# Optimization experiments

Measured on AMD Instinct MI355X. Metric: run time of the kernel, lower is better.

## Reference

```python
import jax, jax.numpy as jnp
import numpy as np

BS, C_IN, L = 64, 64, 4096
C_OUT, KS, K, RATIO = 128, 7, 4, 4
HIDDEN = C_IN // RATIO
PAD, TEMP = 3, 30.0


def setup_inputs() -> dict:
    key = jax.random.key(0)
    k1, k2, k3, k4, k5 = jax.random.split(key, 5)
    x = jax.random.normal(k1, (BS, C_IN, L), dtype=jnp.float32)
    # attention 1x1 convs stored as matmul matrices
    w_attn1 = jax.random.normal(k2, (HIDDEN, C_IN), dtype=jnp.float32) * (2.0 / C_IN) ** 0.5
    w_attn2 = jax.random.normal(k3, (K, HIDDEN), dtype=jnp.float32) * (2.0 / HIDDEN) ** 0.5
    # K-bank conv weights [K, out, in, ks] and biases [K, out]
    weight = jax.random.normal(k4, (K, C_OUT, C_IN, KS), dtype=jnp.float32) * 0.05
    bias = jax.random.normal(k5, (K, C_OUT), dtype=jnp.float32) * 0.05
    return {"x": x, "w_attn1": w_attn1, "w_attn2": w_attn2, "weight": weight, "bias": bias}


def reference(x, w_attn1, w_attn2, weight, bias):
    # Attention1d: global avg pool -> 1x1 conv -> relu -> 1x1 conv -> softmax(./T)
    pooled = jnp.mean(x, axis=-1)                      # [bs, C_in]
    h = jax.nn.relu(pooled @ w_attn1.T)                # [bs, hidden]
    logits = h @ w_attn2.T                             # [bs, K]
    att = jax.nn.softmax(logits / TEMP, axis=-1)       # [bs, K]

    # softmax-weighted aggregation of the K weight banks -> per-sample kernels
    agg_w = jnp.einsum('bk,koif->boif', att, weight)   # [bs, out, in, ks]
    agg_b = att @ bias                                 # [bs, out]

    # per-sample conv1d (the grouped-conv trick), vectorized with vmap
    def conv_one(xi, wi):
        # xi: [C_in, L], wi: [out, in, ks]
        return jax.lax.conv_general_dilated(
            xi[None], wi, window_strides=(1,), padding=[(PAD, PAD)],
            dimension_numbers=('NCH', 'OIH', 'NCH'))[0]  # [out, L]

    out = jax.vmap(conv_one)(x, agg_w) + agg_b[:, :, None]  # [bs, out, L]
    return out
```

## Files before the change

kernel.cpp:

```cpp
#include <hip/hip_runtime.h>

typedef __bf16 bf16;
typedef __bf16 bf16x8 __attribute__((ext_vector_type(8)));
typedef __bf16 bf16x2 __attribute__((ext_vector_type(2)));
typedef float f32x4 __attribute__((ext_vector_type(4)));

#define BS 64
#define CI 64
#define LEN 4096
#define CO 128
#define KS 7
#define NK 4
#define HID 16
#define TEMP 30.0f

#define KTOT 448
#define WROW 456
#define WBAT (CO * WROW)
#define LTILE 128
#define TPB 8
#define XB_ROWS 4112
#define XB_ELE (XB_ROWS * 64)
#define NPART 16

__device__ __forceinline__ void gl_lds16(const void* g, void* l) {
    auto gp = reinterpret_cast<const __attribute__((address_space(1))) unsigned int*>(
        reinterpret_cast<unsigned long long>(g));
    auto lp = reinterpret_cast<__attribute__((address_space(3))) unsigned int*>(
        reinterpret_cast<unsigned long long>(l));
    __builtin_amdgcn_global_load_lds(gp, lp, 16, 0, 0);
}

__global__ __launch_bounds__(256) void trans_kernel(const float* __restrict__ x,
                                                    bf16* __restrict__ xbf,
                                                    float* __restrict__ part) {
    int bid = blockIdx.x;
    int b = bid >> 4, lt = bid & 15;
    int t = threadIdx.x;
    int si = t >> 2, sf = t & 3;
    __shared__ __align__(16) bf16 lds_t[128 * 72];
    __shared__ float lds_red[64 * 4];

    const float* xb = x + (size_t)b * CI * LEN;
    bf16* xo = xbf + (size_t)b * XB_ELE;
    float psum = 0.f;
    int ls0 = lt * 256;

    float4 v0[8], v1[8];
#pragma unroll
    for (int j = 0; j < 8; ++j)
        v0[j] = *(const float4*)(xb + (size_t)si * LEN + ls0 + 4 * (sf + 4 * j));
#pragma unroll
    for (int j = 0; j < 8; ++j)
        v1[j] = *(const float4*)(xb + (size_t)si * LEN + ls0 + 128 + 4 * (sf + 4 * j));

#pragma unroll
    for (int st = 0; st < 2; ++st) {
        const float4* v = st ? v1 : v0;
        int ls = ls0 + st * 128;
#pragma unroll
        for (int j = 0; j < 8; ++j) {
            float4 vv = v[j];
            psum += (vv.x + vv.y) + (vv.z + vv.w);
#pragma unroll
            for (int e = 0; e < 4; ++e)
                lds_t[(4 * (sf + 4 * j) + e) * 72 + si] = (bf16)((&vv.x)[e]);
        }
        __syncthreads();
        int row = t >> 3, l8 = t & 7;
#pragma unroll
        for (int pass = 0; pass < 4; ++pass) {
            int r = pass * 32 + row;
            int gl = ls + r + 8;
            uint4 d = *(const uint4*)((const char*)lds_t + r * 144 + l8 * 16);
            int sw = l8 ^ (gl & 7);
            *(uint4*)((char*)xo + (size_t)gl * 128 + sw * 16) = d;
        }
        if (st == 0) __syncthreads();
    }

    lds_red[si * 4 + sf] = psum;
    __syncthreads();
    if (t < 64)
        part[((size_t)b * NPART + lt) * 64 + t] =
            lds_red[t * 4] + lds_red[t * 4 + 1] + lds_red[t * 4 + 2] + lds_red[t * 4 + 3];

    if (lt == 0 && t < 128) *(uint2*)((char*)xo + t * 8) = make_uint2(0u, 0u);
    if (lt == 15 && t < 128) *(uint2*)((char*)xo + (size_t)4104 * 128 + t * 8) = make_uint2(0u, 0u);
}

__global__ void aggw_kernel(const float* __restrict__ part,
                            const float* __restrict__ w1,
                            const float* __restrict__ w2,
                            const float* __restrict__ weight,
                            float* __restrict__ att_g,
                            bf16* __restrict__ wagg) {
    int o = blockIdx.x >> 1;
    int bh = blockIdx.x & 1;
    int t = threadIdx.x;
    __shared__ float p[32 * 64];
    __shared__ float hsh[32 * 16];
    __shared__ float att_s[32][4];
    __shared__ float lw[4 * KTOT];

    const float* wo = weight + (size_t)o * KTOT;
    for (int idx = t; idx < 4 * KTOT; idx += 256) {
        int bank = idx / KTOT;
        int r = idx - bank * KTOT;
        lw[idx] = wo[(size_t)bank * (CO * KTOT) + r];
    }
    for (int idx = t; idx < 32 * 64; idx += 256) {
        int bb = idx >> 6, i = idx & 63;
        const float* pp = part + ((size_t)(bh * 32 + bb) * NPART) * 64 + i;
        float s = 0.f;
#pragma unroll
        for (int j = 0; j < NPART; ++j) s += pp[j * 64];
        p[idx] = s * (1.0f / LEN);
    }
    __syncthreads();

    {
        int bb = t >> 3, h2 = (t & 7) * 2;
#pragma unroll
        for (int u = 0; u < 2; ++u) {
            int hh = h2 + u;
            float s = 0.f;
            for (int i = 0; i < 64; ++i) s += p[bb * 64 + i] * w1[hh * 64 + i];
            hsh[bb * 16 + hh] = fmaxf(s, 0.f);
        }
    }
    __syncthreads();
    if (t < 32) {
        float lg[NK], m = -1e30f;
#pragma unroll
        for (int k = 0; k < NK; ++k) {
            float s = 0.f;
            for (int j = 0; j < HID; ++j) s += hsh[t * 16 + j] * w2[k * HID + j];
            lg[k] = s * (1.0f / TEMP);
            m = fmaxf(m, lg[k]);
        }
        float e[NK], tot = 0.f;
#pragma unroll
        for (int k = 0; k < NK; ++k) { e[k] = expf(lg[k] - m); tot += e[k]; }
        float inv = 1.0f / tot;
#pragma unroll
        for (int k = 0; k < NK; ++k) {
            att_s[t][k] = e[k] * inv;
            if (blockIdx.x < 2) att_g[(bh * 32 + t) * NK + k] = e[k] * inv;
        }
    }
    __syncthreads();

    if (t < 224) {
        float w8[8];
#pragma unroll
        for (int j = 0; j < 2; ++j) {
            int kout = 2 * t + j;
            int i = kout & 63, f = kout >> 6;
#pragma unroll
            for (int bank = 0; bank < 4; ++bank)
                w8[j * 4 + bank] = lw[bank * KTOT + i * KS + f];
        }
        for (int bb = 0; bb < 32; ++bb) {
            int b = bh * 32 + bb;
            float a0 = att_s[bb][0], a1 = att_s[bb][1];
            float a2 = att_s[bb][2], a3 = att_s[bb][3];
            float v0 = a0 * w8[0] + a1 * w8[1] + a2 * w8[2] + a3 * w8[3];
            float v1 = a0 * w8[4] + a1 * w8[5] + a2 * w8[6] + a3 * w8[7];
            bf16x2 pk; pk[0] = (bf16)v0; pk[1] = (bf16)v1;
            *(bf16x2*)(wagg + (size_t)b * WBAT + o * WROW + 2 * t) = pk;
        }
    }
}

__global__ __launch_bounds__(256, 2) void conv_kernel(
    const bf16* __restrict__ xbf,
    const bf16* __restrict__ wagg,
    const float* __restrict__ att_g,
    const float* __restrict__ bias,
    float* __restrict__ out) {
    __shared__ __align__(1024) bf16 lds_x[2][144 * 64];
    __shared__ float aggb_l[CO];

    int nwg = gridDim.x;
    int bid = blockIdx.x;
    int logical = (bid & 7) * (nwg >> 3) + (bid >> 3);
    int b = logical >> 3;
    int rem = logical & 7;
    int oh = rem >> 2, lsp = rem & 3;

    int t = threadIdx.x;
    int lane = t & 63, wid = t >> 6;
    int ln = lane & 15, g = lane >> 4;
    int wm = wid >> 1, wn = wid & 1;

    if (t < CO) {
        float a0 = att_g[b * NK + 0], a1 = att_g[b * NK + 1];
        float a2 = att_g[b * NK + 2], a3 = att_g[b * NK + 3];
        aggb_l[t] = a0 * bias[0 * CO + t] + a1 * bias[1 * CO + t] +
                    a2 * bias[2 * CO + t] + a3 * bias[3 * CO + t];
    }

    const bf16* wgb = wagg + (size_t)b * WBAT
                    + (size_t)(oh * 64 + wm * 32 + ln) * WROW + g * 8;
    bf16x8 av[2][14];
#pragma unroll
    for (int mf = 0; mf < 2; ++mf)
#pragma unroll
        for (int kk = 0; kk < 14; ++kk)
            av[mf][kk] = *(const bf16x8*)(wgb + mf * 16 * WROW + kk * 32);

    int l0base = lsp * (LTILE * TPB);
    const bf16* xb = xbf + (size_t)b * XB_ELE;

    auto stage = [&](int buf, int l0) {
        const char* src = (const char*)xb + (size_t)l0 * 128 + lane * 16;
        char* dst = (char*)lds_x[buf];
        for (int c = wid; c < 18; c += 4)
            gl_lds16(src + c * 1024, dst + c * 1024);
    };

    stage(0, l0base);
    __syncthreads();

    float bias_r[2][4];
    int orow_off[2][4];
#pragma unroll
    for (int mf = 0; mf < 2; ++mf)
#pragma unroll
        for (int r = 0; r < 4; ++r) {
            int o = oh * 64 + wm * 32 + mf * 16 + g * 4 + r;
            bias_r[mf][r] = aggb_l[o];
            orow_off[mf][r] = (b * CO + o) * LEN;
        }

    int prow = wn * 64 + ln + 5;

    for (int tl = 0; tl < TPB; ++tl) {
        int l0 = l0base + tl * LTILE;
        if (tl + 1 < TPB) stage((tl + 1) & 1, l0 + LTILE);

        f32x4 acc[2][4];
#pragma unroll
        for (int mf = 0; mf < 2; ++mf)
#pragma unroll
            for (int nf = 0; nf < 4; ++nf)
                acc[mf][nf] = (f32x4){0.f, 0.f, 0.f, 0.f};

        const char* lb = (const char*)lds_x[tl & 1];

#pragma unroll
        for (int kk = 0; kk < 14; ++kk) {
            int f = kk >> 1;
            int key = (prow + f) & 7;
            int swz = (((kk & 1) * 4 + g) ^ key) * 16;
            bf16x8 bv[4];
#pragma unroll
            for (int nf = 0; nf < 4; ++nf)
                bv[nf] = *(const bf16x8*)(lb + (prow + nf * 16 + f) * 128 + swz);
#pragma unroll
            for (int mf = 0; mf < 2; ++mf)
#pragma unroll
                for (int nf = 0; nf < 4; ++nf)
                    acc[mf][nf] = __builtin_amdgcn_mfma_f32_16x16x32_bf16(
                        av[mf][kk], bv[nf], acc[mf][nf], 0, 0, 0);
        }

        if (tl + 1 < TPB) __syncthreads();

#pragma unroll
        for (int mf = 0; mf < 2; ++mf)
#pragma unroll
            for (int nf = 0; nf < 4; ++nf) {
                int l = l0 + wn * 64 + nf * 16 + ln;
#pragma unroll
                for (int r = 0; r < 4; ++r)
                    out[(size_t)orow_off[mf][r] + l] = acc[mf][nf][r] + bias_r[mf][r];
            }
    }
}

extern "C" void kernel_launch(void* const* d_in, const int* in_sizes, int n_in,
                              void* d_out, int out_size, void* d_ws, size_t ws_size,
                              hipStream_t stream) {
    const float* x  = (const float*)d_in[0];
    const float* w1 = (const float*)d_in[1];
    const float* w2 = (const float*)d_in[2];
    const float* wt = (const float*)d_in[3];
    const float* bs = (const float*)d_in[4];
    float* out = (float*)d_out;

    bf16* xbf    = (bf16*)d_ws;
    bf16* wagg   = (bf16*)((char*)d_ws + (size_t)BS * XB_ELE * 2);
    float* part  = (float*)((char*)wagg + (size_t)BS * WBAT * 2);
    float* att_g = part + BS * NPART * 64;

    trans_kernel<<<BS * 16, 256, 0, stream>>>(x, xbf, part);
    aggw_kernel<<<CO * 2, 256, 0, stream>>>(part, w1, w2, wt, att_g, wagg);
    conv_kernel<<<BS * 8, 256, 0, stream>>>(xbf, wagg, att_g, bs, out);
}
```

Baseline: 66.85 us.

## Give each wave private LDS double buffers and drop block barriers in conv

Each wave now stages only the input rows it needs (72 rows) into its own double buffer. Completion is tracked with explicit vmcnt waits instead of block-wide __syncthreads, and the bias aggregation moves from shared memory into per-thread registers. The goal is to remove barrier stalls and let waves run independently, at the cost of overlapping halos being loaded twice across waves and a larger LDS footprint (72KB), which may limit occupancy to two blocks per CU. The hand-tuned vmcnt counts must match the exact number of outstanding loads, or the kernel will read incomplete data.

```diff
diff --git a/kernel.cpp b/kernel.cpp
--- a/kernel.cpp
+++ b/kernel.cpp
@@ -17,8 +17,6 @@
 #define KTOT 448
 #define WROW 456
 #define WBAT (CO * WROW)
-#define LTILE 128
-#define TPB 8
 #define XB_ROWS 4112
 #define XB_ELE (XB_ROWS * 64)
 #define NPART 16
@@ -179,8 +177,7 @@
     const float* __restrict__ att_g,
     const float* __restrict__ bias,
     float* __restrict__ out) {
-    __shared__ __align__(1024) bf16 lds_x[2][144 * 64];
-    __shared__ float aggb_l[CO];
+    __shared__ __align__(1024) bf16 lds_x[4][2][4608];
 
     int nwg = gridDim.x;
     int bid = blockIdx.x;
@@ -194,13 +191,6 @@
     int ln = lane & 15, g = lane >> 4;
     int wm = wid >> 1, wn = wid & 1;
 
-    if (t < CO) {
-        float a0 = att_g[b * NK + 0], a1 = att_g[b * NK + 1];
-        float a2 = att_g[b * NK + 2], a3 = att_g[b * NK + 3];
-        aggb_l[t] = a0 * bias[0 * CO + t] + a1 * bias[1 * CO + t] +
-                    a2 * bias[2 * CO + t] + a3 * bias[3 * CO + t];
-    }
-
     const bf16* wgb = wagg + (size_t)b * WBAT
                     + (size_t)(oh * 64 + wm * 32 + ln) * WROW + g * 8;
     bf16x8 av[2][14];
@@ -210,35 +200,45 @@
         for (int kk = 0; kk < 14; ++kk)
             av[mf][kk] = *(const bf16x8*)(wgb + mf * 16 * WROW + kk * 32);
 
-    int l0base = lsp * (LTILE * TPB);
-    const bf16* xb = xbf + (size_t)b * XB_ELE;
-
-    auto stage = [&](int buf, int l0) {
-        const char* src = (const char*)xb + (size_t)l0 * 128 + lane * 16;
-        char* dst = (char*)lds_x[buf];
-        for (int c = wid; c < 18; c += 4)
+    float a0 = att_g[b * NK + 0], a1 = att_g[b * NK + 1];
+    float a2 = att_g[b * NK + 2], a3 = att_g[b * NK + 3];
+    float bias_r[2][4];
+    size_t orow[2][4];
+#pragma unroll
+    for (int mf = 0; mf < 2; ++mf)
+#pragma unroll
+        for (int r = 0; r < 4; ++r) {
+            int o = oh * 64 + wm * 32 + mf * 16 + g * 4 + r;
+            bias_r[mf][r] = a0 * bias[o] + a1 * bias[CO + o] +
+                            a2 * bias[2 * CO + o] + a3 * bias[3 * CO + o];
+            orow[mf][r] = ((size_t)(b * CO + o)) * LEN;
+        }
+
+    int l0base = lsp * 1024;
+    int l0w = l0base + wn * 64;
+    const char* xbb = (const char*)(xbf + (size_t)b * XB_ELE);
+    char* buf0 = (char*)&lds_x[wid][0][0];
+    char* buf1 = (char*)&lds_x[wid][1][0];
+
+    auto stage = [&](char* dst, int gl0) {
+        const char* src = xbb + (size_t)gl0 * 128 + lane * 16;
+#pragma unroll
+        for (int c = 0; c < 9; ++c)
             gl_lds16(src + c * 1024, dst + c * 1024);
     };
 
-    stage(0, l0base);
-    __syncthreads();
-
-    float bias_r[2][4];
-    int orow_off[2][4];
-#pragma unroll
-    for (int mf = 0; mf < 2; ++mf)
-#pragma unroll
-        for (int r = 0; r < 4; ++r) {
-            int o = oh * 64 + wm * 32 + mf * 16 + g * 4 + r;
-            bias_r[mf][r] = aggb_l[o];
-            orow_off[mf][r] = (b * CO + o) * LEN;
-        }
-
-    int prow = wn * 64 + ln + 5;
-
-    for (int tl = 0; tl < TPB; ++tl) {
-        int l0 = l0base + tl * LTILE;
-        if (tl + 1 < TPB) stage((tl + 1) & 1, l0 + LTILE);
+    stage(buf0, l0w + 4);
+
+#pragma unroll
+    for (int tl = 0; tl < 8; ++tl) {
+        char* cur = (tl & 1) ? buf1 : buf0;
+        char* nxt = (tl & 1) ? buf0 : buf1;
+        if (tl + 1 < 8) stage(nxt, l0w + (tl + 1) * 128 + 4);
+
+        if (tl == 0)      asm volatile("s_waitcnt vmcnt(9)" ::: "memory");
+        else if (tl == 7) asm volatile("s_waitcnt vmcnt(32)" ::: "memory");
+        else              asm volatile("s_waitcnt vmcnt(41)" ::: "memory");
+        __builtin_amdgcn_sched_barrier(0);
 
         f32x4 acc[2][4];
 #pragma unroll
@@ -247,17 +247,16 @@
             for (int nf = 0; nf < 4; ++nf)
                 acc[mf][nf] = (f32x4){0.f, 0.f, 0.f, 0.f};
 
-        const char* lb = (const char*)lds_x[tl & 1];
-
 #pragma unroll
         for (int kk = 0; kk < 14; ++kk) {
             int f = kk >> 1;
-            int key = (prow + f) & 7;
-            int swz = (((kk & 1) * 4 + g) ^ key) * 16;
             bf16x8 bv[4];
 #pragma unroll
-            for (int nf = 0; nf < 4; ++nf)
-                bv[nf] = *(const bf16x8*)(lb + (prow + nf * 16 + f) * 128 + swz);
+            for (int nf = 0; nf < 4; ++nf) {
+                int r = nf * 16 + ln + f + 1;
+                int chunk = (((kk & 1) * 4 + g)) ^ ((r + 4) & 7);
+                bv[nf] = *(const bf16x8*)(cur + r * 128 + chunk * 16);
+            }
 #pragma unroll
             for (int mf = 0; mf < 2; ++mf)
 #pragma unroll
@@ -266,8 +265,7 @@
                         av[mf][kk], bv[nf], acc[mf][nf], 0, 0, 0);
         }
 
-        if (tl + 1 < TPB) __syncthreads();
-
+        int l0 = l0base + tl * 128;
 #pragma unroll
         for (int mf = 0; mf < 2; ++mf)
 #pragma unroll
@@ -275,7 +273,7 @@
                 int l = l0 + wn * 64 + nf * 16 + ln;
 #pragma unroll
                 for (int r = 0; r < 4; ++r)
-                    out[(size_t)orow_off[mf][r] + l] = acc[mf][nf][r] + bias_r[mf][r];
+                    out[orow[mf][r] + l] = acc[mf][nf][r] + bias_r[mf][r];
             }
     }
 }
```

New measurement: 68.39 us. 1.02x slower.
